# Optimization experiments

Hardware: AMD Instinct MI355X
Metric: run time of the kernel (lower is better)

Reference implementation:

```python
import jax, jax.numpy as jnp
import numpy as np

ALPHA = 0.25
GAMMA = 2.0
IOU_THRES = 0.5
BETA = 1.0 / 9.0
WEIGHTS = (10.0, 10.0, 10.0, 5.0, 15.0)
DEG2RAD = np.pi / 180.0
EPS = 1e-8
B, A, C, G = 2, 16384, 15, 16


def cross2(u, v):
    return u[..., 0] * v[..., 1] - u[..., 1] * v[..., 0]


def rect_corners(boxes):
    # boxes [..., 5] (cx, cy, w, h, theta_deg) -> corners [..., 4, 2]
    cx, cy, w, h = boxes[..., 0], boxes[..., 1], boxes[..., 2], boxes[..., 3]
    th = boxes[..., 4] * DEG2RAD
    c, s = jnp.cos(th)[..., None], jnp.sin(th)[..., None]
    sx = jnp.asarray([-1.0, 1.0, 1.0, -1.0], boxes.dtype)
    sy = jnp.asarray([-1.0, -1.0, 1.0, 1.0], boxes.dtype)
    dx = 0.5 * w[..., None] * sx
    dy = 0.5 * h[..., None] * sy
    x = cx[..., None] + dx * c - dy * s
    y = cy[..., None] + dx * s + dy * c
    return jnp.stack([x, y], axis=-1)


def points_in_rect(pts, box):
    # pts [..., N, 2], box [..., 5] (broadcastable) -> bool [..., N]
    cx, cy, w, h = box[..., 0:1], box[..., 1:2], box[..., 2:3], box[..., 3:4]
    th = box[..., 4:5] * DEG2RAD
    c, s = jnp.cos(th), jnp.sin(th)
    dx, dy = pts[..., 0] - cx, pts[..., 1] - cy
    lx = dx * c + dy * s
    ly = -dx * s + dy * c
    tol = 1e-4
    return (jnp.abs(lx) <= 0.5 * w + tol) & (jnp.abs(ly) <= 0.5 * h + tol)


def rotated_iou(ab, gb):
    # exact IoU of rotated rects: anchors [A,5] x gts [G,5] -> [A,G]
    ca, cg = rect_corners(ab), rect_corners(gb)              # [A,4,2], [G,4,2]
    a_in_g = points_in_rect(ca[:, None], gb[None, :])        # [A,G,4]
    g_in_a = points_in_rect(cg[None, :], ab[:, None])        # [A,G,4]
    p0 = ca[:, None, :, None]                                # [A,1,4,1,2]
    p1 = jnp.roll(ca, -1, axis=1)[:, None, :, None]
    q0 = cg[None, :, None, :]                                # [1,G,1,4,2]
    q1 = jnp.roll(cg, -1, axis=1)[None, :, None, :]
    d1, d2, r = p1 - p0, q1 - q0, q0 - p0
    den = cross2(d1, d2)                                     # [A,G,4,4]
    safe = jnp.where(jnp.abs(den) < EPS, 1.0, den)
    t = cross2(r, d2) / safe
    u = cross2(r, d1) / safe
    ok = (jnp.abs(den) >= EPS) & (t >= 0.0) & (t <= 1.0) & (u >= 0.0) & (u <= 1.0)
    ipts = p0 + t[..., None] * d1                            # [A,G,4,4,2]
    nA, nG = ab.shape[0], gb.shape[0]
    pts = jnp.concatenate([
        jnp.broadcast_to(ca[:, None], (nA, nG, 4, 2)),
        jnp.broadcast_to(cg[None, :], (nA, nG, 4, 2)),
        ipts.reshape(nA, nG, 16, 2)], axis=2)                # [A,G,24,2]
    msk = jnp.concatenate([a_in_g, g_in_a, ok.reshape(nA, nG, 16)], axis=2)
    cnt = msk.sum(-1)                                        # [A,G]
    mf = msk[..., None].astype(pts.dtype)
    cen = (pts * mf).sum(2) / jnp.maximum(cnt, 1)[..., None]
    rel = (pts - cen[..., None, :]) * mf                     # invalid -> centroid
    ang = jnp.where(msk, jnp.arctan2(rel[..., 1], rel[..., 0]), 1e9)
    order = jnp.argsort(ang, axis=-1)                        # valid verts CCW first
    rel_s = jnp.take_along_axis(rel, order[..., None], axis=2)
    fill = jnp.minimum(jnp.arange(24), jnp.maximum(cnt - 1, 0)[..., None])
    q = jnp.take_along_axis(rel_s, fill[..., None], axis=2)  # tail = last valid vert
    inter = 0.5 * jnp.abs(cross2(q, jnp.roll(q, -1, axis=2)).sum(-1))
    inter = jnp.where(cnt >= 3, inter, 0.0)
    union = (ab[:, 2] * ab[:, 3])[:, None] + (gb[:, 2] * gb[:, 3])[None, :] - inter
    return inter / jnp.maximum(union, EPS)


def square_iou(a, b):
    # IoU of axis-aligned min-area squares (side = max(w,h)), the cheap indicator
    sa = jnp.maximum(a[:, 2], a[:, 3])[:, None] * 0.5
    sb = jnp.maximum(b[:, 2], b[:, 3])[None, :] * 0.5
    ax, ay = a[:, 0:1], a[:, 1:2]
    bx, by = b[:, 0][None, :], b[:, 1][None, :]
    iw = jnp.maximum(jnp.minimum(ax + sa, bx + sb) - jnp.maximum(ax - sa, bx - sb), 0.0)
    ih = jnp.maximum(jnp.minimum(ay + sa, by + sb) - jnp.maximum(ay - sa, by - sb), 0.0)
    inter = iw * ih
    union = 4.0 * sa * sa + 4.0 * sb * sb - inter
    return inter / jnp.maximum(union, EPS)


def encode(ex, gt):
    # BoxCoder.encode, weights (10,10,10,5,15), xywht with tan(theta) delta
    ew = jnp.maximum(ex[..., 2], 1.0)
    eh = jnp.maximum(ex[..., 3], 1.0)
    gw = jnp.maximum(gt[..., 2], 1.0)
    gh = jnp.maximum(gt[..., 3], 1.0)
    wx, wy, ww, wh, wt = WEIGHTS
    dx = wx * (gt[..., 0] - ex[..., 0]) / ew
    dy = wy * (gt[..., 1] - ex[..., 1]) / eh
    dw = ww * jnp.log(gw / ew)
    dh = wh * jnp.log(gh / eh)
    dt = wt * (jnp.tan(gt[..., 4] * DEG2RAD) - jnp.tan(ex[..., 4] * DEG2RAD))
    return jnp.stack([dx, dy, dw, dh, dt], axis=-1)


def image_loss(cls_p, reg_p, anc, ann):
    labels = ann[:, 5]
    valid_g = labels != -1.0
    has_gt = valid_g.any()
    p = jnp.clip(cls_p, 1e-4, 1.0 - 1e-4)
    # IoU assignment is detached in the original (numpy round-trip)
    anc_sg = jax.lax.stop_gradient(anc)
    gt_sg = jax.lax.stop_gradient(ann[:, :5])
    ind = square_iou(anc_sg, gt_sg)
    iou = jnp.where(ind > 0.1, rotated_iou(anc_sg, gt_sg), 0.0)
    iou = jnp.where(valid_g[None, :], iou, -1.0)             # mask padded gts
    iou_max, iou_arg = iou.max(1), iou.argmax(1)             # per anchor
    pos = iou_max >= IOU_THRES
    max_gt, arg_gt = iou.max(0), iou.argmax(0)               # per gt
    force = (valid_g & (max_gt < IOU_THRES)).astype(jnp.int32)
    pos = pos | (jnp.zeros((anc.shape[0],), jnp.int32).at[arg_gt].max(force) > 0)
    assigned = ann[iou_arg]                                  # [A,6]
    onehot = jax.nn.one_hot(assigned[:, 5].astype(jnp.int32), cls_p.shape[1], dtype=p.dtype)
    tgt = jnp.full_like(p, -1.0)
    tgt = jnp.where((iou_max < IOU_THRES - 0.1)[:, None], 0.0, tgt)
    tgt = jnp.where(pos[:, None], onehot, tgt)
    num_pos = pos.sum()
    af = jnp.where(tgt == 1.0, ALPHA, 1.0 - ALPHA)
    fw = af * jnp.where(tgt == 1.0, 1.0 - p, p) ** GAMMA
    bce = -(tgt * jnp.log(p + 1e-6) + (1.0 - tgt) * jnp.log(1.0 - p + 1e-6))
    cls_loss = jnp.where(tgt != -1.0, fw * bce, 0.0).sum() / jnp.maximum(num_pos.astype(p.dtype), 1.0)
    reg_t = encode(anc, assigned[:, :5])
    diff = jnp.abs(reg_p - reg_t)
    sl1 = jnp.where(diff < BETA, 0.5 * diff * diff / BETA, diff - 0.5 * BETA)
    denom = jnp.maximum(num_pos * 5, 1).astype(p.dtype)      # .mean() over [num_pos,5]
    reg_loss = jnp.where(num_pos > 0, jnp.where(pos[:, None], sl1, 0.0).sum() / denom, 0.0)
    return jnp.where(has_gt, cls_loss, 0.0), jnp.where(has_gt, reg_loss, 0.0)


def setup_inputs():
    key = jax.random.key(0)
    k1, k2, k3, k4, k5, k6, k7 = jax.random.split(key, 7)
    classifications = jax.random.uniform(k1, (B, A, C), jnp.float32, 0.01, 0.99)
    regressions = jax.random.normal(k2, (B, A, 5), jnp.float32) * 0.1
    ctr = jax.random.uniform(k3, (B, A, 2), jnp.float32, 0.0, 1024.0)
    wh = jax.random.uniform(k4, (B, A, 2), jnp.float32, 16.0, 256.0)
    th = jax.random.uniform(k5, (B, A, 1), jnp.float32, -45.0, 45.0)
    anchors = jnp.concatenate([ctr, wh, th], axis=-1)
    gctr = jax.random.uniform(k6, (B, G, 2), jnp.float32, 100.0, 900.0)
    gwh = jax.random.uniform(k7, (B, G, 2), jnp.float32, 30.0, 300.0)
    gth = jax.random.uniform(jax.random.fold_in(key, 1), (B, G, 1), jnp.float32, -45.0, 45.0)
    lab = jax.random.randint(jax.random.fold_in(key, 2), (B, G, 1), 0, C).astype(jnp.float32)
    lab = lab.at[:, -4:, :].set(-1.0)  # padded gts (label == -1 sentinel)
    annotations = jnp.concatenate([gctr, gwh, gth, lab], axis=-1)
    return {"classifications": classifications, "regressions": regressions,
            "anchors": anchors, "annotations": annotations}


def reference(classifications, regressions, anchors, annotations):
    cls_l, reg_l = jax.vmap(image_loss)(classifications, regressions, anchors, annotations)
    return (jnp.mean(cls_l, keepdims=True), jnp.mean(reg_l, keepdims=True))
```

## Files before the change

### kernel.cpp

```cpp
#include <hip/hip_runtime.h>

#define B_ 2
#define A_ 16384
#define C_ 15
#define G_ 16
#define D2Rf 0.017453292519943295f
#define ENC_HALF 0xBF000000u
#define ENC_04   0xBECCCCCDu
#define NSEG 128
#define HB_ 256
#define HT_ 128
#define LB_ 128
#define SEGCAP 4096
#define OSTR 25

__device__ __forceinline__ unsigned enc_f32(float f) {
    unsigned u = __float_as_uint(f);
    return u ^ ((u >> 31) ? 0xFFFFFFFFu : 0x80000000u);
}

__device__ __forceinline__ float pseudo_angle(float y, float x) {
    float d = fabsf(x) + fabsf(y);
    float r = y / d;
    float p = (x >= 0.f) ? r : ((y >= 0.f) ? 2.f - r : -2.f - r);
    return (d == 0.f) ? 0.f : p;
}

__device__ __forceinline__ void rect_corners5(const float* b, float X[4], float Y[4],
                                              float* cth, float* sth) {
    float th = b[4] * D2Rf;
    float c = cosf(th), s = sinf(th);
    *cth = c; *sth = s;
    const float SX[4] = {-1.f, 1.f, 1.f, -1.f};
    const float SY[4] = {-1.f, -1.f, 1.f, 1.f};
    float hw = 0.5f * b[2], hh = 0.5f * b[3];
#pragma unroll
    for (int i = 0; i < 4; ++i) {
        float dx = hw * SX[i];
        float dy = hh * SY[i];
        X[i] = b[0] + dx * c - dy * s;
        Y[i] = b[1] + dx * s + dy * c;
    }
}

__device__ __forceinline__ float rotated_iou_pair(const float* ab, const float* gb,
                                                  float* ox, float* oy) {
    float ax[4], ay[4], gx[4], gy[4];
    float cA, sA, cG, sG;
    rect_corners5(ab, ax, ay, &cA, &sA);
    rect_corners5(gb, gx, gy, &cG, &sG);

    float rx[24], ry[24];
    unsigned msk = 0u;

#pragma unroll
    for (int i = 0; i < 4; ++i) {
        float dx = ax[i] - gb[0], dy = ay[i] - gb[1];
        float lx = dx * cG + dy * sG;
        float ly = -dx * sG + dy * cG;
        bool in = (fabsf(lx) <= 0.5f * gb[2] + 1e-4f) && (fabsf(ly) <= 0.5f * gb[3] + 1e-4f);
        rx[i] = ax[i]; ry[i] = ay[i];
        if (in) msk |= (1u << i);
    }
#pragma unroll
    for (int i = 0; i < 4; ++i) {
        float dx = gx[i] - ab[0], dy = gy[i] - ab[1];
        float lx = dx * cA + dy * sA;
        float ly = -dx * sA + dy * cA;
        bool in = (fabsf(lx) <= 0.5f * ab[2] + 1e-4f) && (fabsf(ly) <= 0.5f * ab[3] + 1e-4f);
        rx[4 + i] = gx[i]; ry[4 + i] = gy[i];
        if (in) msk |= (1u << (4 + i));
    }
#pragma unroll
    for (int i = 0; i < 4; ++i) {
        float p0x = ax[i], p0y = ay[i];
        float p1x = ax[(i + 1) & 3], p1y = ay[(i + 1) & 3];
        float d1x = p1x - p0x, d1y = p1y - p0y;
#pragma unroll
        for (int j = 0; j < 4; ++j) {
            float q0x = gx[j], q0y = gy[j];
            float q1x = gx[(j + 1) & 3], q1y = gy[(j + 1) & 3];
            float d2x = q1x - q0x, d2y = q1y - q0y;
            float rrx = q0x - p0x, rry = q0y - p0y;
            float den = d1x * d2y - d1y * d2x;
            float safe = (fabsf(den) < 1e-8f) ? 1.f : den;
            float t = (rrx * d2y - rry * d2x) / safe;
            float u = (rrx * d1y - rry * d1x) / safe;
            bool ok = (fabsf(den) >= 1e-8f) && (t >= 0.f) && (t <= 1.f) && (u >= 0.f) && (u <= 1.f);
            int k = 8 + i * 4 + j;
            rx[k] = p0x + t * d1x;
            ry[k] = p0y + t * d1y;
            if (ok) msk |= (1u << k);
        }
    }

    int cnt = __popc(msk);
    float sx = 0.f, sy = 0.f;
#pragma unroll
    for (int k = 0; k < 24; ++k)
        if ((msk >> k) & 1u) { sx += rx[k]; sy += ry[k]; }
    float cnf = fmaxf((float)cnt, 1.f);
    float cenx = sx / cnf, ceny = sy / cnf;

    const unsigned long long UNM = ((unsigned long long)enc_f32(1e9f)) << 5;
    unsigned long long kk[24];
#pragma unroll
    for (int k = 0; k < 24; ++k) {
        if ((msk >> k) & 1u) {
            rx[k] -= cenx; ry[k] -= ceny;
            kk[k] = (((unsigned long long)enc_f32(pseudo_angle(ry[k], rx[k]))) << 5)
                    | (unsigned)k;
        } else {
            kk[k] = UNM | (unsigned)k;
        }
    }

    int rnk[24];
#pragma unroll
    for (int k = 0; k < 24; ++k) {
        int r = 0;
#pragma unroll
        for (int j = 0; j < 24; ++j)
            r += (kk[j] < kk[k]) ? 1 : 0;
        rnk[k] = r;
    }

#pragma unroll
    for (int k = 0; k < 24; ++k) {
        if ((msk >> k) & 1u) { ox[rnk[k]] = rx[k]; oy[rnk[k]] = ry[k]; }
    }

    float inter = 0.f;
    if (cnt >= 3) {
        float x0 = ox[0], y0 = oy[0];
        float xp = x0, yp = y0, ssum = 0.f;
        for (int r = 1; r < cnt; ++r) {
            float xc = ox[r], yc = oy[r];
            ssum += xp * yc - yp * xc;
            xp = xc; yp = yc;
        }
        ssum += xp * y0 - yp * x0;
        inter = 0.5f * fabsf(ssum);
    }
    float uni = ab[2] * ab[3] + gb[2] * gb[3] - inter;
    return inter / fmaxf(uni, 1e-8f);
}

__global__ void __launch_bounds__(256, 1)
gate_kernel(const float* __restrict__ anc,
            const float* __restrict__ ann,
            unsigned long long* __restrict__ rowMaxArg,
            unsigned* __restrict__ seg,
            unsigned* __restrict__ segcnt,
            unsigned* __restrict__ ctr) {
    __shared__ int ss[256];
    const int tid = threadIdx.x;
    const int t = blockIdx.x * 256 + tid;
    const int b = blockIdx.x >> 6;

    if (blockIdx.x == 0 && tid == 0) ctr[0] = 0u;

    const float* ab = anc + (size_t)t * 5;
    float a0 = ab[0], a1 = ab[1], a2 = ab[2], a3 = ab[3];
    float sa = 0.5f * fmaxf(a2, a3);

    unsigned passmask = 0u;
    unsigned long long rk = 0ull;
#pragma unroll
    for (int g = 0; g < G_; ++g) {
        const float* gb = ann + ((size_t)b * G_ + g) * 6;
        float v;
        if (gb[5] == -1.0f) {
            v = -1.0f;
        } else {
            float sb = 0.5f * fmaxf(gb[2], gb[3]);
            float iw = fminf(a0 + sa, gb[0] + sb) - fmaxf(a0 - sa, gb[0] - sb);
            iw = fmaxf(iw, 0.f);
            float ih = fminf(a1 + sa, gb[1] + sb) - fmaxf(a1 - sa, gb[1] - sb);
            ih = fmaxf(ih, 0.f);
            float inter = iw * ih;
            float uni = 4.f * sa * sa + 4.f * sb * sb - inter;
            float ind = inter / fmaxf(uni, 1e-8f);
            if (ind > 0.1f) passmask |= (1u << g);
            v = 0.f;
        }
        unsigned long long key =
            ((unsigned long long)enc_f32(v) << 32) | (unsigned)(G_ - 1 - g);
        if (key > rk) rk = key;
    }
    rowMaxArg[t] = rk;

    int cnt = __popc(passmask);
    ss[tid] = cnt;
    __syncthreads();
    for (int s = 1; s < 256; s <<= 1) {
        int v = (tid >= s) ? ss[tid - s] : 0;
        __syncthreads();
        ss[tid] += v;
        __syncthreads();
    }
    unsigned p = (unsigned)(ss[tid] - cnt);
    unsigned* mySeg = seg + (size_t)blockIdx.x * SEGCAP;
#pragma unroll
    for (int g = 0; g < G_; ++g) {
        if ((passmask >> g) & 1u) mySeg[p++] = ((unsigned)tid << 4) | (unsigned)g;
    }
    if (tid == 0) segcnt[blockIdx.x] = (unsigned)ss[255];
}

__global__ void __launch_bounds__(HT_, 1)
heavy_kernel(const float* __restrict__ anc,
             const float* __restrict__ ann,
             const unsigned* __restrict__ seg,
             const unsigned* __restrict__ segcnt,
             unsigned long long* __restrict__ rowMaxArg,
             unsigned long long* __restrict__ partials) {
    __shared__ unsigned inc[NSEG];
    __shared__ unsigned long long cells[32];
    __shared__ float ordx[HT_ * OSTR];
    __shared__ float ordy[HT_ * OSTR];
    const int tid = threadIdx.x;
    float* ox = ordx + tid * OSTR;
    float* oy = ordy + tid * OSTR;

    if (tid < 32) cells[tid] = 0ull;
    inc[tid] = segcnt[tid];
    __syncthreads();
    for (int s = 1; s < NSEG; s <<= 1) {
        unsigned v = (tid >= s) ? inc[tid - s] : 0u;
        __syncthreads();
        inc[tid] += v;
        __syncthreads();
    }
    const unsigned n = inc[NSEG - 1];

    for (unsigned i = (unsigned)(blockIdx.x * HT_ + tid); i < n; i += HB_ * HT_) {
        int lo = 0, hi = NSEG - 1;
        while (lo < hi) {
            int mid = (lo + hi) >> 1;
            if (inc[mid] > i) hi = mid; else lo = mid + 1;
        }
        unsigned base = (lo == 0) ? 0u : inc[lo - 1];
        unsigned e = seg[(size_t)lo * SEGCAP + (i - base)];
        int t2 = lo * 256 + (int)(e >> 4);
        int g = (int)(e & 15u);
        int b2 = t2 >> 14;
        const float* ab2 = anc + (size_t)t2 * 5;
        const float* gb2 = ann + ((size_t)b2 * G_ + g) * 6;
        float v = rotated_iou_pair(ab2, gb2, ox, oy);
        unsigned long long ev = (unsigned long long)enc_f32(v);
        atomicMax(&rowMaxArg[t2], (ev << 32) | (unsigned)(G_ - 1 - g));
        int aIdx = t2 & (A_ - 1);
        atomicMax(&cells[b2 * G_ + g], (ev << 32) | (0xFFFFFFFFu - (unsigned)aIdx));
    }
    __syncthreads();
    if (tid < 32) partials[(size_t)blockIdx.x * 32 + tid] = cells[tid];
}

__global__ void __launch_bounds__(256, 1)
loss_kernel(const float* __restrict__ cls_p,
            const float* __restrict__ reg_p,
            const float* __restrict__ anc,
            const float* __restrict__ ann,
            const unsigned long long* __restrict__ rowMaxArg,
            const unsigned long long* __restrict__ partials,
            float* __restrict__ pcls,
            float* __restrict__ preg,
            int* __restrict__ pnp,
            unsigned* __restrict__ ctr,
            float* __restrict__ out) {
    __shared__ unsigned long long red[256];
    __shared__ unsigned long long pk32[32];
    __shared__ float sc[256], sr[256];
    __shared__ int sp[256];
    __shared__ int lastFlag;

    const int tid = threadIdx.x;

    {
        int cell = tid & 31, chunk = tid >> 5;
        unsigned long long m = 0ull;
        for (int blk = chunk * (HB_ / 8); blk < (chunk + 1) * (HB_ / 8); ++blk) {
            unsigned long long v = partials[(size_t)blk * 32 + cell];
            if (v > m) m = v;
        }
        red[tid] = m;
    }
    __syncthreads();
    if (tid < 32) {
        unsigned long long mm =
            ((unsigned long long)enc_f32(0.0f) << 32) | 0xFFFFFFFFu;
        for (int c = 0; c < 8; ++c) {
            unsigned long long v = red[c * 32 + tid];
            if (v > mm) mm = v;
        }
        pk32[tid] = mm;
    }
    __syncthreads();

    const int t = blockIdx.x * 256 + tid;
    const int b = t >> 14;
    const int a = t & (A_ - 1);

    unsigned long long rk = rowMaxArg[t];
    unsigned ehi = (unsigned)(rk >> 32);
    int arg = (G_ - 1) - (int)(rk & 0xFu);

    bool forcedf = false;
#pragma unroll
    for (int g = 0; g < G_; ++g) {
        unsigned long long pkv = pk32[b * G_ + g];
        float lab = ann[((size_t)b * G_ + g) * 6 + 5];
        unsigned hi = (unsigned)(pkv >> 32);
        unsigned ai = 0xFFFFFFFFu - (unsigned)pkv;
        forcedf |= (lab != -1.0f) && (hi < ENC_HALF) && (ai == (unsigned)a);
    }

    bool pos = (ehi >= ENC_HALF) || forcedf;
    const float* g6 = ann + ((size_t)b * G_ + arg) * 6;
    int cls = (int)g6[5];

    float csum = 0.f;
    if (pos || ehi < ENC_04) {
        const float* pr = cls_p + (size_t)t * C_;
#pragma unroll
        for (int c = 0; c < C_; ++c) {
            float tgt = (pos && c == cls) ? 1.f : 0.f;
            float pv = fminf(fmaxf(pr[c], 1e-4f), 1.f - 1e-4f);
            float af = (tgt == 1.f) ? 0.25f : 0.75f;
            float x = (tgt == 1.f) ? (1.f - pv) : pv;
            float fw = af * x * x;
            float bce = -(tgt * logf(pv + 1e-6f) + (1.f - tgt) * logf(1.f - pv + 1e-6f));
            csum += fw * bce;
        }
    }

    float rsum = 0.f;
    if (pos) {
        const float* ex = anc + (size_t)t * 5;
        const float* rp = reg_p + (size_t)t * 5;
        float ew = fmaxf(ex[2], 1.f), eh2 = fmaxf(ex[3], 1.f);
        float gw = fmaxf(g6[2], 1.f), gh = fmaxf(g6[3], 1.f);
        float tg[5];
        tg[0] = 10.f * (g6[0] - ex[0]) / ew;
        tg[1] = 10.f * (g6[1] - ex[1]) / eh2;
        tg[2] = 10.f * logf(gw / ew);
        tg[3] = 5.f * logf(gh / eh2);
        tg[4] = 15.f * (tanf(g6[4] * D2Rf) - tanf(ex[4] * D2Rf));
        const float BETAf = (float)(1.0 / 9.0);
#pragma unroll
        for (int i = 0; i < 5; ++i) {
            float d = fabsf(rp[i] - tg[i]);
            rsum += (d < BETAf) ? 0.5f * d * d / BETAf : d - 0.5f * BETAf;
        }
    }

    sc[tid] = csum; sr[tid] = rsum; sp[tid] = pos ? 1 : 0;
    __syncthreads();
    for (int s = 128; s > 0; s >>= 1) {
        if (tid < s) {
            sc[tid] += sc[tid + s];
            sr[tid] += sr[tid + s];
            sp[tid] += sp[tid + s];
        }
        __syncthreads();
    }
    if (tid == 0) {
        pcls[blockIdx.x] = sc[0];
        preg[blockIdx.x] = sr[0];
        pnp[blockIdx.x] = sp[0];
        __threadfence();
        unsigned v = atomicAdd(ctr, 1u);
        lastFlag = (v == (unsigned)(LB_ - 1));
    }
    __syncthreads();

    if (lastFlag) {
        __threadfence();
        if (tid < LB_) {
            sc[tid] = pcls[tid];
            sr[tid] = preg[tid];
            sp[tid] = pnp[tid];
        }
        __syncthreads();
        if (tid == 0) {
            const int BPI = LB_ / B_;
            float cm = 0.f, rm = 0.f;
            for (int bb = 0; bb < B_; ++bb) {
                float cs = 0.f, rs = 0.f; int np = 0;
                for (int i = 0; i < BPI; ++i) {
                    cs += sc[bb * BPI + i];
                    rs += sr[bb * BPI + i];
                    np += sp[bb * BPI + i];
                }
                bool has = false;
                for (int g = 0; g < G_; ++g)
                    if (ann[((size_t)bb * G_ + g) * 6 + 5] != -1.0f) has = true;
                float c_ = cs / fmaxf((float)np, 1.f);
                int d5 = np * 5; if (d5 < 1) d5 = 1;
                float r_ = (np > 0) ? rs / (float)d5 : 0.f;
                cm += has ? c_ : 0.f;
                rm += has ? r_ : 0.f;
            }
            out[0] = cm / (float)B_;
            out[1] = rm / (float)B_;
        }
    }
}

extern "C" void kernel_launch(void* const* d_in, const int* in_sizes, int n_in,
                              void* d_out, int out_size, void* d_ws, size_t ws_size,
                              hipStream_t stream) {
    const float* cls_p = (const float*)d_in[0];
    const float* reg_p = (const float*)d_in[1];
    const float* anc   = (const float*)d_in[2];
    const float* ann   = (const float*)d_in[3];
    float* out = (float*)d_out;

    char* ws = (char*)d_ws;
    unsigned* ctrp = (unsigned*)ws;
    unsigned long long* rowMaxArg = (unsigned long long*)(ws + 256);
    unsigned long long* partials = rowMaxArg + (size_t)B_ * A_;
    unsigned* segcnt = (unsigned*)(partials + (size_t)HB_ * 32);
    unsigned* seg    = segcnt + NSEG;
    float* pcls = (float*)(seg + (size_t)NSEG * SEGCAP);
    float* preg = pcls + LB_;
    int*   pnp  = (int*)(preg + LB_);

    gate_kernel<<<NSEG, 256, 0, stream>>>(anc, ann, rowMaxArg, seg, segcnt, ctrp);
    heavy_kernel<<<HB_, HT_, 0, stream>>>(anc, ann, seg, segcnt, rowMaxArg, partials);
    loss_kernel<<<LB_, 256, 0, stream>>>(cls_p, reg_p, anc, ann, rowMaxArg,
                                         partials, pcls, preg, pnp, ctrp, out);
}
```

Baseline: 38.20 us.

## Fuse gate and heavy IoU kernels with block-local candidate lists

Merges the AABB gating kernel and the rotated-IoU kernel into a single kernel. Each block gates 128 anchors, compacts the passing pairs into a shared-memory list, and evaluates them with 256 threads, using shared atomics for the row max and per-gt max. This removes one launch, the global segment buffers, the binary search and the global atomics. It also halves the rank comparisons by using symmetric pairwise counting. The cost is possible load imbalance across blocks, since work is no longer spread globally.

```diff
diff --git a/kernel.cpp b/kernel.cpp
--- a/kernel.cpp
+++ b/kernel.cpp
@@ -7,11 +7,9 @@
 #define D2Rf 0.017453292519943295f
 #define ENC_HALF 0xBF000000u
 #define ENC_04   0xBECCCCCDu
-#define NSEG 128
-#define HB_ 256
-#define HT_ 128
+#define K1B 256
+#define K1T 256
 #define LB_ 128
-#define SEGCAP 4096
 #define OSTR 25
 
 __device__ __forceinline__ unsigned enc_f32(float f) {
@@ -117,12 +115,15 @@
 
     int rnk[24];
 #pragma unroll
-    for (int k = 0; k < 24; ++k) {
-        int r = 0;
-#pragma unroll
-        for (int j = 0; j < 24; ++j)
-            r += (kk[j] < kk[k]) ? 1 : 0;
-        rnk[k] = r;
+    for (int k = 0; k < 24; ++k) rnk[k] = 0;
+#pragma unroll
+    for (int k = 1; k < 24; ++k) {
+#pragma unroll
+        for (int j = 0; j < k; ++j) {
+            bool c = kk[j] < kk[k];
+            rnk[k] += c ? 1 : 0;
+            rnk[j] += c ? 0 : 1;
+        }
     }
 
 #pragma unroll
@@ -146,115 +147,94 @@
     return inter / fmaxf(uni, 1e-8f);
 }
 
-__global__ void __launch_bounds__(256, 1)
-gate_kernel(const float* __restrict__ anc,
-            const float* __restrict__ ann,
-            unsigned long long* __restrict__ rowMaxArg,
-            unsigned* __restrict__ seg,
-            unsigned* __restrict__ segcnt,
-            unsigned* __restrict__ ctr) {
-    __shared__ int ss[256];
+__global__ void __launch_bounds__(K1T, 1)
+gate_heavy_kernel(const float* __restrict__ anc,
+                  const float* __restrict__ ann,
+                  unsigned long long* __restrict__ rowMaxArg,
+                  unsigned long long* __restrict__ partials,
+                  unsigned* __restrict__ ctr) {
+    __shared__ unsigned long long rowkey[128];
+    __shared__ unsigned long long cells[16];
+    __shared__ unsigned short list[2048];
+    __shared__ int ss[128];
+    __shared__ float ordx[K1T * OSTR];
+    __shared__ float ordy[K1T * OSTR];
+
     const int tid = threadIdx.x;
-    const int t = blockIdx.x * 256 + tid;
-    const int b = blockIdx.x >> 6;
-
-    if (blockIdx.x == 0 && tid == 0) ctr[0] = 0u;
-
-    const float* ab = anc + (size_t)t * 5;
-    float a0 = ab[0], a1 = ab[1], a2 = ab[2], a3 = ab[3];
-    float sa = 0.5f * fmaxf(a2, a3);
-
-    unsigned passmask = 0u;
-    unsigned long long rk = 0ull;
-#pragma unroll
-    for (int g = 0; g < G_; ++g) {
-        const float* gb = ann + ((size_t)b * G_ + g) * 6;
-        float v;
-        if (gb[5] == -1.0f) {
-            v = -1.0f;
-        } else {
-            float sb = 0.5f * fmaxf(gb[2], gb[3]);
-            float iw = fminf(a0 + sa, gb[0] + sb) - fmaxf(a0 - sa, gb[0] - sb);
-            iw = fmaxf(iw, 0.f);
-            float ih = fminf(a1 + sa, gb[1] + sb) - fmaxf(a1 - sa, gb[1] - sb);
-            ih = fmaxf(ih, 0.f);
-            float inter = iw * ih;
-            float uni = 4.f * sa * sa + 4.f * sb * sb - inter;
-            float ind = inter / fmaxf(uni, 1e-8f);
-            if (ind > 0.1f) passmask |= (1u << g);
-            v = 0.f;
-        }
-        unsigned long long key =
-            ((unsigned long long)enc_f32(v) << 32) | (unsigned)(G_ - 1 - g);
-        if (key > rk) rk = key;
-    }
-    rowMaxArg[t] = rk;
-
-    int cnt = __popc(passmask);
-    ss[tid] = cnt;
-    __syncthreads();
-    for (int s = 1; s < 256; s <<= 1) {
-        int v = (tid >= s) ? ss[tid - s] : 0;
-        __syncthreads();
-        ss[tid] += v;
-        __syncthreads();
-    }
-    unsigned p = (unsigned)(ss[tid] - cnt);
-    unsigned* mySeg = seg + (size_t)blockIdx.x * SEGCAP;
-#pragma unroll
-    for (int g = 0; g < G_; ++g) {
-        if ((passmask >> g) & 1u) mySeg[p++] = ((unsigned)tid << 4) | (unsigned)g;
-    }
-    if (tid == 0) segcnt[blockIdx.x] = (unsigned)ss[255];
-}
-
-__global__ void __launch_bounds__(HT_, 1)
-heavy_kernel(const float* __restrict__ anc,
-             const float* __restrict__ ann,
-             const unsigned* __restrict__ seg,
-             const unsigned* __restrict__ segcnt,
-             unsigned long long* __restrict__ rowMaxArg,
-             unsigned long long* __restrict__ partials) {
-    __shared__ unsigned inc[NSEG];
-    __shared__ unsigned long long cells[32];
-    __shared__ float ordx[HT_ * OSTR];
-    __shared__ float ordy[HT_ * OSTR];
-    const int tid = threadIdx.x;
+    const int blk = blockIdx.x;
+    const int b = blk >> 7;
     float* ox = ordx + tid * OSTR;
     float* oy = ordy + tid * OSTR;
 
-    if (tid < 32) cells[tid] = 0ull;
-    inc[tid] = segcnt[tid];
-    __syncthreads();
-    for (int s = 1; s < NSEG; s <<= 1) {
-        unsigned v = (tid >= s) ? inc[tid - s] : 0u;
+    if (blk == 0 && tid == 0) ctr[0] = 0u;
+    if (tid < 16) cells[tid] = 0ull;
+
+    unsigned passmask = 0u;
+    if (tid < 128) {
+        const int t = blk * 128 + tid;
+        const float* ab = anc + (size_t)t * 5;
+        float a0 = ab[0], a1 = ab[1];
+        float sa = 0.5f * fmaxf(ab[2], ab[3]);
+        unsigned long long rk = 0ull;
+#pragma unroll
+        for (int g = 0; g < G_; ++g) {
+            const float* gb = ann + ((size_t)b * G_ + g) * 6;
+            float v;
+            if (gb[5] == -1.0f) {
+                v = -1.0f;
+            } else {
+                float sb = 0.5f * fmaxf(gb[2], gb[3]);
+                float iw = fminf(a0 + sa, gb[0] + sb) - fmaxf(a0 - sa, gb[0] - sb);
+                iw = fmaxf(iw, 0.f);
+                float ih = fminf(a1 + sa, gb[1] + sb) - fmaxf(a1 - sa, gb[1] - sb);
+                ih = fmaxf(ih, 0.f);
+                float inter = iw * ih;
+                float uni = 4.f * sa * sa + 4.f * sb * sb - inter;
+                float ind = inter / fmaxf(uni, 1e-8f);
+                if (ind > 0.1f) passmask |= (1u << g);
+                v = 0.f;
+            }
+            unsigned long long key =
+                ((unsigned long long)enc_f32(v) << 32) | (unsigned)(G_ - 1 - g);
+            if (key > rk) rk = key;
+        }
+        rowkey[tid] = rk;
+        ss[tid] = __popc(passmask);
+    }
+    __syncthreads();
+
+    for (int s = 1; s < 128; s <<= 1) {
+        int v = (tid < 128 && tid >= s) ? ss[tid - s] : 0;
         __syncthreads();
-        inc[tid] += v;
+        if (tid < 128) ss[tid] += v;
         __syncthreads();
     }
-    const unsigned n = inc[NSEG - 1];
-
-    for (unsigned i = (unsigned)(blockIdx.x * HT_ + tid); i < n; i += HB_ * HT_) {
-        int lo = 0, hi = NSEG - 1;
-        while (lo < hi) {
-            int mid = (lo + hi) >> 1;
-            if (inc[mid] > i) hi = mid; else lo = mid + 1;
-        }
-        unsigned base = (lo == 0) ? 0u : inc[lo - 1];
-        unsigned e = seg[(size_t)lo * SEGCAP + (i - base)];
-        int t2 = lo * 256 + (int)(e >> 4);
-        int g = (int)(e & 15u);
-        int b2 = t2 >> 14;
-        const float* ab2 = anc + (size_t)t2 * 5;
-        const float* gb2 = ann + ((size_t)b2 * G_ + g) * 6;
-        float v = rotated_iou_pair(ab2, gb2, ox, oy);
+    if (tid < 128) {
+        unsigned p = (unsigned)(ss[tid] - __popc(passmask));
+#pragma unroll
+        for (int g = 0; g < G_; ++g) {
+            if ((passmask >> g) & 1u)
+                list[p++] = (unsigned short)(((unsigned)tid << 4) | (unsigned)g);
+        }
+    }
+    __syncthreads();
+    const unsigned n = (unsigned)ss[127];
+
+    for (unsigned i = (unsigned)tid; i < n; i += K1T) {
+        unsigned e = (unsigned)list[i];
+        int la = (int)(e >> 4), g = (int)(e & 15u);
+        int t2 = blk * 128 + la;
+        float v = rotated_iou_pair(anc + (size_t)t2 * 5,
+                                   ann + ((size_t)b * G_ + g) * 6, ox, oy);
         unsigned long long ev = (unsigned long long)enc_f32(v);
-        atomicMax(&rowMaxArg[t2], (ev << 32) | (unsigned)(G_ - 1 - g));
-        int aIdx = t2 & (A_ - 1);
-        atomicMax(&cells[b2 * G_ + g], (ev << 32) | (0xFFFFFFFFu - (unsigned)aIdx));
-    }
-    __syncthreads();
-    if (tid < 32) partials[(size_t)blockIdx.x * 32 + tid] = cells[tid];
+        atomicMax(&rowkey[la], (ev << 32) | (unsigned)(G_ - 1 - g));
+        unsigned aIdx = (unsigned)(t2 & (A_ - 1));
+        atomicMax(&cells[g], (ev << 32) | (0xFFFFFFFFu - aIdx));
+    }
+    __syncthreads();
+
+    if (tid < 128) rowMaxArg[blk * 128 + tid] = rowkey[tid];
+    if (tid < 16) partials[(size_t)blk * 16 + tid] = cells[tid];
 }
 
 __global__ void __launch_bounds__(256, 1)
@@ -278,22 +258,18 @@
     const int tid = threadIdx.x;
 
     {
-        int cell = tid & 31, chunk = tid >> 5;
+        int cc = tid >> 3, sub = tid & 7;
+        int b3 = cc >> 4, g3 = cc & 15;
         unsigned long long m = 0ull;
-        for (int blk = chunk * (HB_ / 8); blk < (chunk + 1) * (HB_ / 8); ++blk) {
-            unsigned long long v = partials[(size_t)blk * 32 + cell];
-            if (v > m) m = v;
-        }
+        for (int k = sub; k < 128; k += 8)
+            m = max(m, partials[(size_t)(b3 * 128 + k) * 16 + g3]);
         red[tid] = m;
     }
     __syncthreads();
     if (tid < 32) {
         unsigned long long mm =
             ((unsigned long long)enc_f32(0.0f) << 32) | 0xFFFFFFFFu;
-        for (int c = 0; c < 8; ++c) {
-            unsigned long long v = red[c * 32 + tid];
-            if (v > mm) mm = v;
-        }
+        for (int j = 0; j < 8; ++j) mm = max(mm, red[tid * 8 + j]);
         pk32[tid] = mm;
     }
     __syncthreads();
@@ -421,14 +397,11 @@
     unsigned* ctrp = (unsigned*)ws;
     unsigned long long* rowMaxArg = (unsigned long long*)(ws + 256);
     unsigned long long* partials = rowMaxArg + (size_t)B_ * A_;
-    unsigned* segcnt = (unsigned*)(partials + (size_t)HB_ * 32);
-    unsigned* seg    = segcnt + NSEG;
-    float* pcls = (float*)(seg + (size_t)NSEG * SEGCAP);
+    float* pcls = (float*)(partials + (size_t)K1B * 16);
     float* preg = pcls + LB_;
     int*   pnp  = (int*)(preg + LB_);
 
-    gate_kernel<<<NSEG, 256, 0, stream>>>(anc, ann, rowMaxArg, seg, segcnt, ctrp);
-    heavy_kernel<<<HB_, HT_, 0, stream>>>(anc, ann, seg, segcnt, rowMaxArg, partials);
+    gate_heavy_kernel<<<K1B, K1T, 0, stream>>>(anc, ann, rowMaxArg, partials, ctrp);
     loss_kernel<<<LB_, 256, 0, stream>>>(cls_p, reg_p, anc, ann, rowMaxArg,
                                          partials, pcls, preg, pnp, ctrp, out);
 }
```

New measurement: 39.57 us. +3.6%, slower.

## Replace rotated IoU vertex sort with Sutherland-Hodgman polygon clipping

Applied to the files above, without the earlier changes.

Computes the intersection polygon of two rotated rectangles by clipping the anchor quad against each of the four gt edges (Sutherland-Hodgman), instead of gathering 24 candidate points, computing pseudo-angles and ranking them with an O(24^2) compare sort. This removes the candidate generation, the 16 segment-intersection divisions and the ranking work in the heavy kernel, and uses ping-pong shared-memory buffers of 9 slots per thread. Results can differ slightly from the reference near degenerate or touching configurations, because the reference's 1e-4 containment tolerance and EPS handling are not reproduced, and the inner loop has a data-dependent trip count.

```diff
diff --git a/kernel.cpp b/kernel.cpp
--- a/kernel.cpp
+++ b/kernel.cpp
@@ -12,25 +12,16 @@
 #define HT_ 128
 #define LB_ 128
 #define SEGCAP 4096
-#define OSTR 25
+#define PSTR 9
 
 __device__ __forceinline__ unsigned enc_f32(float f) {
     unsigned u = __float_as_uint(f);
     return u ^ ((u >> 31) ? 0xFFFFFFFFu : 0x80000000u);
 }
 
-__device__ __forceinline__ float pseudo_angle(float y, float x) {
-    float d = fabsf(x) + fabsf(y);
-    float r = y / d;
-    float p = (x >= 0.f) ? r : ((y >= 0.f) ? 2.f - r : -2.f - r);
-    return (d == 0.f) ? 0.f : p;
-}
-
-__device__ __forceinline__ void rect_corners5(const float* b, float X[4], float Y[4],
-                                              float* cth, float* sth) {
+__device__ __forceinline__ void rect_corners4(const float* b, float X[4], float Y[4]) {
     float th = b[4] * D2Rf;
     float c = cosf(th), s = sinf(th);
-    *cth = c; *sth = s;
     const float SX[4] = {-1.f, 1.f, 1.f, -1.f};
     const float SY[4] = {-1.f, -1.f, 1.f, 1.f};
     float hw = 0.5f * b[2], hh = 0.5f * b[3];
@@ -44,98 +35,51 @@
 }
 
 __device__ __forceinline__ float rotated_iou_pair(const float* ab, const float* gb,
-                                                  float* ox, float* oy) {
+                                                  float* PX, float* PY,
+                                                  float* QX, float* QY) {
     float ax[4], ay[4], gx[4], gy[4];
-    float cA, sA, cG, sG;
-    rect_corners5(ab, ax, ay, &cA, &sA);
-    rect_corners5(gb, gx, gy, &cG, &sG);
-
-    float rx[24], ry[24];
-    unsigned msk = 0u;
-
-#pragma unroll
-    for (int i = 0; i < 4; ++i) {
-        float dx = ax[i] - gb[0], dy = ay[i] - gb[1];
-        float lx = dx * cG + dy * sG;
-        float ly = -dx * sG + dy * cG;
-        bool in = (fabsf(lx) <= 0.5f * gb[2] + 1e-4f) && (fabsf(ly) <= 0.5f * gb[3] + 1e-4f);
-        rx[i] = ax[i]; ry[i] = ay[i];
-        if (in) msk |= (1u << i);
-    }
-#pragma unroll
-    for (int i = 0; i < 4; ++i) {
-        float dx = gx[i] - ab[0], dy = gy[i] - ab[1];
-        float lx = dx * cA + dy * sA;
-        float ly = -dx * sA + dy * cA;
-        bool in = (fabsf(lx) <= 0.5f * ab[2] + 1e-4f) && (fabsf(ly) <= 0.5f * ab[3] + 1e-4f);
-        rx[4 + i] = gx[i]; ry[4 + i] = gy[i];
-        if (in) msk |= (1u << (4 + i));
-    }
-#pragma unroll
-    for (int i = 0; i < 4; ++i) {
-        float p0x = ax[i], p0y = ay[i];
-        float p1x = ax[(i + 1) & 3], p1y = ay[(i + 1) & 3];
-        float d1x = p1x - p0x, d1y = p1y - p0y;
-#pragma unroll
-        for (int j = 0; j < 4; ++j) {
-            float q0x = gx[j], q0y = gy[j];
-            float q1x = gx[(j + 1) & 3], q1y = gy[(j + 1) & 3];
-            float d2x = q1x - q0x, d2y = q1y - q0y;
-            float rrx = q0x - p0x, rry = q0y - p0y;
-            float den = d1x * d2y - d1y * d2x;
-            float safe = (fabsf(den) < 1e-8f) ? 1.f : den;
-            float t = (rrx * d2y - rry * d2x) / safe;
-            float u = (rrx * d1y - rry * d1x) / safe;
-            bool ok = (fabsf(den) >= 1e-8f) && (t >= 0.f) && (t <= 1.f) && (u >= 0.f) && (u <= 1.f);
-            int k = 8 + i * 4 + j;
-            rx[k] = p0x + t * d1x;
-            ry[k] = p0y + t * d1y;
-            if (ok) msk |= (1u << k);
-        }
-    }
-
-    int cnt = __popc(msk);
-    float sx = 0.f, sy = 0.f;
-#pragma unroll
-    for (int k = 0; k < 24; ++k)
-        if ((msk >> k) & 1u) { sx += rx[k]; sy += ry[k]; }
-    float cnf = fmaxf((float)cnt, 1.f);
-    float cenx = sx / cnf, ceny = sy / cnf;
-
-    const unsigned long long UNM = ((unsigned long long)enc_f32(1e9f)) << 5;
-    unsigned long long kk[24];
-#pragma unroll
-    for (int k = 0; k < 24; ++k) {
-        if ((msk >> k) & 1u) {
-            rx[k] -= cenx; ry[k] -= ceny;
-            kk[k] = (((unsigned long long)enc_f32(pseudo_angle(ry[k], rx[k]))) << 5)
-                    | (unsigned)k;
-        } else {
-            kk[k] = UNM | (unsigned)k;
-        }
-    }
-
-    int rnk[24];
-#pragma unroll
-    for (int k = 0; k < 24; ++k) {
-        int r = 0;
-#pragma unroll
-        for (int j = 0; j < 24; ++j)
-            r += (kk[j] < kk[k]) ? 1 : 0;
-        rnk[k] = r;
-    }
-
-#pragma unroll
-    for (int k = 0; k < 24; ++k) {
-        if ((msk >> k) & 1u) { ox[rnk[k]] = rx[k]; oy[rnk[k]] = ry[k]; }
+    rect_corners4(ab, ax, ay);
+    rect_corners4(gb, gx, gy);
+
+#pragma unroll
+    for (int i = 0; i < 4; ++i) { PX[i] = ax[i]; PY[i] = ay[i]; }
+    int n = 4;
+
+    float* px = PX; float* py = PY;
+    float* qx = QX; float* qy = QY;
+
+#pragma unroll
+    for (int j = 0; j < 4; ++j) {
+        float e0x = gx[j], e0y = gy[j];
+        float ex = gx[(j + 1) & 3] - e0x;
+        float ey = gy[(j + 1) & 3] - e0y;
+        int m = 0;
+        float sxv = px[n - 1], syv = py[n - 1];
+        float ss = ex * (syv - e0y) - ey * (sxv - e0x);
+        for (int i = 0; i < n; ++i) {
+            float exv = px[i], eyv = py[i];
+            float se = ex * (eyv - e0y) - ey * (exv - e0x);
+            if ((ss >= 0.f) != (se >= 0.f)) {
+                float tpar = ss / (ss - se);
+                qx[m] = sxv + tpar * (exv - sxv);
+                qy[m] = syv + tpar * (eyv - syv);
+                ++m;
+            }
+            if (se >= 0.f) { qx[m] = exv; qy[m] = eyv; ++m; }
+            sxv = exv; syv = eyv; ss = se;
+        }
+        n = m;
+        float* tx = px; px = qx; qx = tx;
+        float* ty = py; py = qy; qy = ty;
+        if (n == 0) break;
     }
 
     float inter = 0.f;
-    if (cnt >= 3) {
-        float x0 = ox[0], y0 = oy[0];
+    if (n >= 3) {
+        float x0 = px[0], y0 = py[0];
         float xp = x0, yp = y0, ssum = 0.f;
-        for (int r = 1; r < cnt; ++r) {
-            float xc = ox[r], yc = oy[r];
+        for (int r = 1; r < n; ++r) {
+            float xc = px[r], yc = py[r];
             ssum += xp * yc - yp * xc;
             xp = xc; yp = yc;
         }
@@ -217,11 +161,15 @@
              unsigned long long* __restrict__ partials) {
     __shared__ unsigned inc[NSEG];
     __shared__ unsigned long long cells[32];
-    __shared__ float ordx[HT_ * OSTR];
-    __shared__ float ordy[HT_ * OSTR];
+    __shared__ float bufPX[HT_ * PSTR];
+    __shared__ float bufPY[HT_ * PSTR];
+    __shared__ float bufQX[HT_ * PSTR];
+    __shared__ float bufQY[HT_ * PSTR];
     const int tid = threadIdx.x;
-    float* ox = ordx + tid * OSTR;
-    float* oy = ordy + tid * OSTR;
+    float* PX = bufPX + tid * PSTR;
+    float* PY = bufPY + tid * PSTR;
+    float* QX = bufQX + tid * PSTR;
+    float* QY = bufQY + tid * PSTR;
 
     if (tid < 32) cells[tid] = 0ull;
     inc[tid] = segcnt[tid];
@@ -247,7 +195,7 @@
         int b2 = t2 >> 14;
         const float* ab2 = anc + (size_t)t2 * 5;
         const float* gb2 = ann + ((size_t)b2 * G_ + g) * 6;
-        float v = rotated_iou_pair(ab2, gb2, ox, oy);
+        float v = rotated_iou_pair(ab2, gb2, PX, PY, QX, QY);
         unsigned long long ev = (unsigned long long)enc_f32(v);
         atomicMax(&rowMaxArg[t2], (ev << 32) | (unsigned)(G_ - 1 - g));
         int aIdx = t2 & (A_ - 1);
```

Result: faster. 32.07 us (-16.0%).
